# Optimization experiments

Measured on AMD Instinct MI355X. Metric: run time of the kernel, lower is better.

## Reference

```python
import jax, jax.numpy as jnp
import numpy as np

B, H, LB, PW, TC = 4096, 64, 32, 16, 1
WL = LB + PW  # window_length = look_back + prediction


def setup_inputs() -> dict:
    key = jax.random.key(0)
    ks = jax.random.split(key, 9)
    bnd = 1.0 / np.sqrt(H)  # torch Linear default init bound
    bnd_h = 1.0 / np.sqrt(H)
    return {
        "x": jax.random.normal(ks[0], (B, LB, TC), jnp.float32),
        "F_w": jax.random.uniform(ks[1], (WL, H, H), jnp.float32, -bnd, bnd),
        "F_b": jax.random.uniform(ks[2], (WL, H), jnp.float32, -bnd, bnd),
        "H_w": jax.random.uniform(ks[3], (WL, TC, H), jnp.float32, -bnd_h, bnd_h),
        "H_b": jax.random.uniform(ks[4], (WL, TC), jnp.float32, -bnd_h, bnd_h),
        "initial_state": jax.random.normal(ks[5], (H,), jnp.float32),
        "initial_covariance": 0.1 * jax.random.normal(ks[6], (H, H), jnp.float32),
        "Q": 0.1 * jax.random.normal(ks[7], (H, H), jnp.float32),
        "R": jnp.eye(TC, dtype=jnp.float32) + 0.1 * jax.random.normal(ks[8], (TC, TC), jnp.float32),
    }


def _kalman_forward(x, F_w, F_b, H_w, H_b, s0, P0, Q, R):
    nb = x.shape[0]
    hs = jnp.broadcast_to(s0, (nb, H))          # (B,H)
    P = jnp.broadcast_to(P0, (nb, H, H))        # (B,H,H)
    ys = jnp.moveaxis(x[:, :LB, :TC], 0, 1)     # (LB,B,TC) per-step observations

    @jax.checkpoint
    def kf_step(carry, inp):
        hs, P = carry
        Fw, Fb, Hw, Hb, y = inp
        hs_pred = hs @ Fw.T + Fb                                        # (B,H)
        P_pred = jnp.einsum('ij,bjk,lk->bil', Fw, P, Fw) + Q            # F P F^T + Q
        resid = y - (hs_pred @ Hw.T + Hb)                               # (B,TC)
        S = jnp.einsum('ij,bjk,lk->bil', Hw, P_pred, Hw) + R            # (B,TC,TC)
        K = jnp.einsum('bij,kj->bik', P_pred, Hw) @ jnp.linalg.inv(S)   # (B,H,TC)
        hs_new = hs_pred + jnp.einsum('bij,bj->bi', K, resid)
        P_new = P_pred - jnp.einsum('bit,tj,bjk->bik', K, Hw, P_pred)   # (I-KH)P_pred
        return (hs_new, P_new), None

    (hs, _), _ = jax.lax.scan(
        kf_step, (hs, P), (F_w[:LB], F_b[:LB], H_w[:LB], H_b[:LB], ys))

    def pred_step(hs, inp):
        Fw, Fb, Hw, Hb = inp
        hs = hs @ Fw.T + Fb
        return hs, hs @ Hw.T + Hb

    _, ems = jax.lax.scan(
        pred_step, hs, (F_w[LB:], F_b[LB:], H_w[LB:], H_b[LB:]))  # (PW,B,TC)
    # torch.cat(preds, dim=1).unsqueeze(-1) -> (B, PW*TC, 1)
    return jnp.moveaxis(ems, 0, 1).reshape(nb, PW * TC)[..., None]


def reference(x, F_w, F_b, H_w, H_b, initial_state, initial_covariance, Q, R):
    return _kalman_forward(x, F_w, F_b, H_w, H_b, initial_state, initial_covariance, Q, R)
```

## Files before the change

kernel.cpp:

```cpp
#include <hip/hip_runtime.h>


constexpr int KP_OFF = 0;
constexpr int WP_OFF = 2048;
constexpr int UP_OFF = 4160;
constexpr int EP_OFF = 5184;
constexpr int WS_U64 = 5200;

typedef float    f32x4 __attribute__((ext_vector_type(4)));
typedef _Float16 f16x4 __attribute__((ext_vector_type(4)));
typedef _Float16 f16x8 __attribute__((ext_vector_type(8)));

#define MFMA16(a, b, c) __builtin_amdgcn_mfma_f32_16x16x16f16((a), (b), (c), 0, 0, 0)

template <int CTRL>
__device__ __forceinline__ float dpp_add(float x) {
  int v = __builtin_amdgcn_update_dpp(0, __builtin_bit_cast(int, x), CTRL, 0xf, 0xf, true);
  return x + __builtin_bit_cast(float, v);
}
__device__ __forceinline__ float sum16(float x) {
  x = dpp_add<0xB1>(x);
  x = dpp_add<0x4E>(x);
  x = dpp_add<0x141>(x);
  x = dpp_add<0x140>(x);
  return x;
}
__device__ __forceinline__ float sum64(float x) {
  x = sum16(x);
  x += __shfl_xor(x, 16, 64);
  x += __shfl_xor(x, 32, 64);
  return x;
}

__device__ __forceinline__ float spin_read(const unsigned long long* p, unsigned tag) {
  unsigned long long v = 0;
  for (int it = 0; it < (1 << 22); ++it) {
    v = __hip_atomic_load(p, __ATOMIC_RELAXED, __HIP_MEMORY_SCOPE_AGENT);
    if ((unsigned)(v >> 32) == tag) break;
  }
  union { unsigned u; float f; } cv; cv.u = (unsigned)v;
  return cv.f;
}
__device__ __forceinline__ void pub_write(unsigned long long* p, unsigned tag, float x) {
  union { float f; unsigned u; } cv; cv.f = x;
  __hip_atomic_store(p, ((unsigned long long)tag << 32) | cv.u,
                     __ATOMIC_RELAXED, __HIP_MEMORY_SCOPE_AGENT);
}

__global__ __launch_bounds__(512) void kalman_fused(
    const float* __restrict__ Fw, const float* __restrict__ Fb,
    const float* __restrict__ Hw, const float* __restrict__ Hb,
    const float* __restrict__ s0, const float* __restrict__ P0,
    const float* __restrict__ Qg, const float* __restrict__ Rg,
    const float* __restrict__ x, float* __restrict__ out,
    unsigned long long* __restrict__ ws) {
  __shared__ __align__(16) char smem[55040];
  const int tid  = threadIdx.x;
  const int lane = tid & 63;
  const int w    = tid >> 6;
  const int blk  = blockIdx.x;
  unsigned long long* kp = ws + KP_OFF;
  unsigned long long* wp = ws + WP_OFF;
  unsigned long long* up = ws + UP_OFF;
  unsigned long long* ep = ws + EP_OFF;

  if (blk == 0) {
    _Float16* FF  = (_Float16*)smem;
    _Float16* TF  = (_Float16*)(smem + 16640);
    float*    PF  = (float*)(smem + 33024);
    float*    nred = (float*)(smem + 53504);
    float*    mred = (float*)(smem + 54016);

    const int l15 = lane & 15, g = lane >> 4;
    const int ti = w >> 1, half = w & 1;
    const int lp0 = 16 * (l15 >> 2) + 4 * g;
    const int rg  = l15 & 3;
    const int sr = tid >> 3, sc0 = (tid & 7) * 8;
    const int fi = (sr >> 4) * 4 + (sc0 >> 4);
    const int L0 = (sr & 15) + 16 * ((sc0 >> 2) & 3);
    const float R0 = Rg[0];

    auto FFp = [&](int f, int l) { return FF + (f * 65 + l) * 8; };
    auto TFp = [&](int f, int l) { return TF + (f * 64 + l) * 8; };
    auto PFi = [&](int f, int l, int r) { return (f * 64 + l) * 5 + r; };

    auto stageF = [&](f32x4 a, f32x4 b) {
      f16x8 pa, pb;
      #pragma unroll
      for (int u = 0; u < 4; ++u) {
        const _Float16 ha = (_Float16)a[u];
        pa[u] = ha; pa[4 + u] = (_Float16)((a[u] - (float)ha) * 2048.0f);
        const _Float16 hb = (_Float16)b[u];
        pb[u] = hb; pb[4 + u] = (_Float16)((b[u] - (float)hb) * 2048.0f);
      }
      *(f16x8*)FFp(fi, L0)      = pa;
      *(f16x8*)FFp(fi, L0 + 16) = pb;
    };

    float qf0[4], qf1[4];
    #pragma unroll
    for (int reg = 0; reg < 4; ++reg) {
      qf0[reg] = Qg[(16 * ti + 4 * g + reg) * 64 + 16 * (2 * half) + l15];
      qf1[reg] = Qg[(16 * ti + 4 * g + reg) * 64 + 16 * (2 * half + 1) + l15];
    }
    #pragma unroll
    for (int u = 0; u < 8; ++u) {
      const int cc = sc0 + u;
      PF[PFi((sr >> 4) * 4 + (cc >> 4), 16 * ((sr & 15) >> 2) + (cc & 15), sr & 3)] =
          P0[sr * 64 + cc];
    }
    f32x4 fpa = *(const f32x4*)(Fw + sr * 64 + sc0);
    f32x4 fpb = *(const f32x4*)(Fw + sr * 64 + sc0 + 4);
    stageF(fpa, fpb);
    float hcur = Hw[lane], hprev = 0.f, hnext = 0.f;
    __syncthreads();

    for (int t = 0; t < 32; ++t) {
      float kv = 0.f, mr = 0.f;
      if (t > 0) {
        const float n = nred[lane] + nred[64 + lane];
        mr = mred[lane] + mred[64 + lane] + mred[128 + lane] + mred[192 + lane];
        const float s = sum64(hprev * n);
        kv = n / (s + R0);
        if (w == 0) pub_write(&kp[(t - 1) * 64 + lane], (unsigned)t, kv);
      }
      if (t + 1 < 32) {
        fpa = *(const f32x4*)(Fw + (size_t)(t + 1) * 4096 + sr * 64 + sc0);
        fpb = *(const f32x4*)(Fw + (size_t)(t + 1) * 4096 + sr * 64 + sc0 + 4);
        hnext = Hw[(t + 1) * 64 + lane];
      }
      const float kr = __shfl(kv, l15 + 16 * ti, 64);
      f16x4 Ah[4], Al[4];
      #pragma unroll
      for (int kc = 0; kc < 4; ++kc) {
        #pragma unroll
        for (int j = 0; j < 4; ++j) {
          const float mcol = __shfl(mr, 16 * kc + 4 * g + j, 64);
          const float pv = PF[PFi(ti * 4 + kc, lp0 + j, rg)] - kr * mcol;
          const _Float16 hi_ = (_Float16)pv;
          Ah[kc][j] = hi_;
          Al[kc][j] = (_Float16)((pv - (float)hi_) * 2048.0f);
        }
      }
      f16x4 FAh[4], FAl[4];
      #pragma unroll
      for (int kc = 0; kc < 4; ++kc) {
        const f16x8 av = *(const f16x8*)FFp(ti * 4 + kc, lane);
        FAh[kc] = __builtin_shufflevector(av, av, 0, 1, 2, 3);
        FAl[kc] = __builtin_shufflevector(av, av, 4, 5, 6, 7);
      }
      #pragma unroll
      for (int s2 = 0; s2 < 2; ++s2) {
        const int tj = 2 * half + s2;
        f32x4 am = {0.f, 0.f, 0.f, 0.f}, a1 = {0.f, 0.f, 0.f, 0.f}, a2 = {0.f, 0.f, 0.f, 0.f};
        #pragma unroll
        for (int kc = 0; kc < 4; ++kc) {
          const f16x8 bv = *(const f16x8*)FFp(tj * 4 + kc, lane);
          const f16x4 bh = __builtin_shufflevector(bv, bv, 0, 1, 2, 3);
          const f16x4 bl = __builtin_shufflevector(bv, bv, 4, 5, 6, 7);
          am = MFMA16(Ah[kc], bh, am);
          a1 = MFMA16(Ah[kc], bl, a1);
          a2 = MFMA16(Al[kc], bh, a2);
        }
        const f32x4 outv = am + (a1 + a2) * (1.0f / 2048.0f);
        f16x8 tv;
        #pragma unroll
        for (int j = 0; j < 4; ++j) {
          const _Float16 hi_ = (_Float16)outv[j];
          tv[j] = hi_;
          tv[4 + j] = (_Float16)((outv[j] - (float)hi_) * 2048.0f);
        }
        *(f16x8*)TFp(ti * 4 + tj, lane) = tv;
      }
      __syncthreads();

      if (t + 1 < 32) stageF(fpa, fpb);
      f32x4 pout[2];
      #pragma unroll
      for (int s2 = 0; s2 < 2; ++s2) {
        const int tj = 2 * half + s2;
        f32x4 am = {0.f, 0.f, 0.f, 0.f}, a1 = {0.f, 0.f, 0.f, 0.f}, a2 = {0.f, 0.f, 0.f, 0.f};
        #pragma unroll
        for (int kc = 0; kc < 4; ++kc) {
          const f16x8 bv = *(const f16x8*)TFp(kc * 4 + tj, lane);
          const f16x4 bh = __builtin_shufflevector(bv, bv, 0, 1, 2, 3);
          const f16x4 bl = __builtin_shufflevector(bv, bv, 4, 5, 6, 7);
          am = MFMA16(FAh[kc], bh, am);
          a1 = MFMA16(FAh[kc], bl, a1);
          a2 = MFMA16(FAl[kc], bh, a2);
        }
        pout[s2] = am + (a1 + a2) * (1.0f / 2048.0f);
        #pragma unroll
        for (int reg = 0; reg < 4; ++reg) {
          pout[s2][reg] += (s2 ? qf1[reg] : qf0[reg]);
          PF[PFi(ti * 4 + tj, lane, reg)] = pout[s2][reg];
        }
      }
      const float hcA = __shfl(hcur, 16 * (2 * half) + l15, 64);
      const float hcB = __shfl(hcur, 16 * (2 * half + 1) + l15, 64);
      float hr[4];
      #pragma unroll
      for (int reg = 0; reg < 4; ++reg) hr[reg] = __shfl(hcur, 16 * ti + 4 * g + reg, 64);
      #pragma unroll
      for (int reg = 0; reg < 4; ++reg) {
        float np = pout[0][reg] * hcA + pout[1][reg] * hcB;
        np = sum16(np);
        if (l15 == 0) nred[half * 64 + 16 * ti + 4 * g + reg] = np;
      }
      float mp0 = 0.f, mp1 = 0.f;
      #pragma unroll
      for (int reg = 0; reg < 4; ++reg) {
        mp0 += pout[0][reg] * hr[reg];
        mp1 += pout[1][reg] * hr[reg];
      }
      mp0 += __shfl_xor(mp0, 16, 64); mp0 += __shfl_xor(mp0, 32, 64);
      mp1 += __shfl_xor(mp1, 16, 64); mp1 += __shfl_xor(mp1, 32, 64);
      if (g == 0) {
        mred[ti * 64 + 16 * (2 * half) + l15]     = mp0;
        mred[ti * 64 + 16 * (2 * half + 1) + l15] = mp1;
      }
      __syncthreads();
      hprev = hcur; hcur = hnext;
    }
    {
      const float n = nred[lane] + nred[64 + lane];
      const float s = sum64(hprev * n);
      if (w == 0) pub_write(&kp[31 * 64 + lane], 32u, n / (s + R0));
    }
    return;
  }

  if (blk == 1) {
    for (int pi = 0; pi < 2; ++pi) {
      const int p = pi ? (15 - w) : w;
      const int q = 32 + p;
      float r = Hw[q * 64 + lane];
      float eacc = 0.f;
      for (int s = 0; s <= p; ++s) {
        const int m = q - s;
        eacc += r * Fb[m * 64 + lane];
        const float* Fm = Fw + (size_t)m * 4096;
        float r0 = 0.f, r1 = 0.f, r2 = 0.f, r3 = 0.f;
        for (int j = 0; j < 64; j += 4) {
          r0 += __shfl(r, j,     64) * Fm[j * 64 + lane];
          r1 += __shfl(r, j + 1, 64) * Fm[(j + 1) * 64 + lane];
          r2 += __shfl(r, j + 2, 64) * Fm[(j + 2) * 64 + lane];
          r3 += __shfl(r, j + 3, 64) * Fm[(j + 3) * 64 + lane];
        }
        r = (r0 + r1) + (r2 + r3);
      }
      eacc = sum64(eacc);
      pub_write(&up[p * 64 + lane], 1u, r);
      if (lane == 0) pub_write(&ep[p], 1u, eacc + Hb[q]);
    }
    return;
  }

  if (blk < 7) {
    float* vb = (float*)smem + w * 64;
    const int c = (blk - 2) * 8 + w;
    if (c > 32) return;
    if (c == 32) {
      pub_write(&wp[32 * 64 + lane], 1u, spin_read(&kp[31 * 64 + lane], 32u));
      return;
    }
    const int t0 = (c == 0) ? 0 : c;
    float v = (c == 0) ? s0[lane] : spin_read(&kp[(c - 1) * 64 + lane], (unsigned)c);
    f32x4 fn[16];
    {
      const float* Fr = Fw + (size_t)t0 * 4096 + lane * 64;
      #pragma unroll
      for (int jc = 0; jc < 16; ++jc) fn[jc] = *(const f32x4*)(Fr + jc * 4);
    }
    float hn  = Hw[t0 * 64 + lane];
    float fbn = (c == 0) ? Fb[t0 * 64 + lane] : 0.f;
    for (int t = t0; t < 32; ++t) {
      vb[lane] = v;
      f32x4 fc[16];
      #pragma unroll
      for (int jc = 0; jc < 16; ++jc) fc[jc] = fn[jc];
      const float ht = hn, fbt = fbn;
      if (t + 1 < 32) {
        const float* Fr = Fw + (size_t)(t + 1) * 4096 + lane * 64;
        #pragma unroll
        for (int jc = 0; jc < 16; ++jc) fn[jc] = *(const f32x4*)(Fr + jc * 4);
        hn = Hw[(t + 1) * 64 + lane];
        if (c == 0) fbn = Fb[(t + 1) * 64 + lane];
      }
      float a0 = fbt, a1 = 0.f, a2 = 0.f, a3 = 0.f;
      #pragma unroll
      for (int jc = 0; jc < 16; ++jc) {
        const f32x4 vv = *(const f32x4*)(vb + jc * 4);
        a0 += fc[jc].x * vv.x; a1 += fc[jc].y * vv.y;
        a2 += fc[jc].z * vv.z; a3 += fc[jc].w * vv.w;
      }
      const float vp = (a0 + a1) + (a2 + a3);
      float hv = sum64(ht * vp);
      if (c == 0) hv += Hb[t];
      const float kt = spin_read(&kp[t * 64 + lane], (unsigned)(t + 1));
      v = vp - kt * hv;
    }
    pub_write(&wp[c * 64 + lane], 1u, v);
    return;
  }

  {
    float* Ul = (float*)smem;
    float* Wl = (float*)(smem + 4352);
    float* Zl = (float*)(smem + 13328);
    float* El = (float*)(smem + 15504);
    for (int idx = tid; idx < 1024; idx += 512)
      Ul[(idx >> 6) * 68 + (idx & 63)] = spin_read(&up[idx], 1u);
    for (int idx = tid; idx < 2112; idx += 512)
      Wl[(idx >> 6) * 68 + (idx & 63)] = spin_read(&wp[idx], 1u);
    if (tid < 16) El[tid] = spin_read(&ep[tid], 1u);
    __syncthreads();
    for (int idx = tid; idx < 528; idx += 512) {
      const int p = idx / 33, cc = idx - p * 33;
      const float* Up = Ul + p * 68;
      const float* Wc = Wl + cc * 68;
      float a0 = 0.f, a1 = 0.f, a2 = 0.f, a3 = 0.f;
      #pragma unroll 4
      for (int i = 0; i < 64; i += 4) {
        a0 += Up[i] * Wc[i];     a1 += Up[i + 1] * Wc[i + 1];
        a2 += Up[i + 2] * Wc[i + 2]; a3 += Up[i + 3] * Wc[i + 3];
      }
      float z = (a0 + a1) + (a2 + a3);
      if (cc == 0) z += El[p];
      Zl[p * 34 + cc] = z;
    }
    const int b = (blk - 7) * 512 + tid;
    f32x4 xr[8];
    const f32x4* xp = (const f32x4*)(x + (size_t)b * 32);
    #pragma unroll
    for (int u = 0; u < 8; ++u) xr[u] = xp[u];
    __syncthreads();
    float acc[16];
    #pragma unroll
    for (int p = 0; p < 16; ++p) acc[p] = Zl[p * 34];
    #pragma unroll
    for (int u = 0; u < 8; ++u) {
      #pragma unroll
      for (int e = 0; e < 4; ++e) {
        const float xval = xr[u][e];
        const int t = u * 4 + e;
        #pragma unroll
        for (int p = 0; p < 16; ++p) acc[p] += Zl[p * 34 + 1 + t] * xval;
      }
    }
    float4* op = (float4*)(out + (size_t)b * 16);
    op[0] = make_float4(acc[0], acc[1], acc[2], acc[3]);
    op[1] = make_float4(acc[4], acc[5], acc[6], acc[7]);
    op[2] = make_float4(acc[8], acc[9], acc[10], acc[11]);
    op[3] = make_float4(acc[12], acc[13], acc[14], acc[15]);
  }
}

extern "C" void kernel_launch(void* const* d_in, const int* in_sizes, int n_in,
                              void* d_out, int out_size, void* d_ws, size_t ws_size,
                              hipStream_t stream) {
  (void)in_sizes; (void)n_in; (void)out_size; (void)ws_size;
  const float* x  = (const float*)d_in[0];
  const float* Fw = (const float*)d_in[1];
  const float* Fb = (const float*)d_in[2];
  const float* Hw = (const float*)d_in[3];
  const float* Hb = (const float*)d_in[4];
  const float* s0 = (const float*)d_in[5];
  const float* P0 = (const float*)d_in[6];
  const float* Q  = (const float*)d_in[7];
  const float* R  = (const float*)d_in[8];
  float* out = (float*)d_out;
  unsigned long long* ws = (unsigned long long*)d_ws;

  hipMemsetAsync(d_ws, 0, WS_U64 * sizeof(unsigned long long), stream);
  kalman_fused<<<15, 512, 0, stream>>>(Fw, Fb, Hw, Hb, s0, P0, Q, R, x, out, ws);
}
```

Measured before the change: 127.7 us.

## Fold per-column state recurrence into covariance block via MFMA, drop cross-block spin

Moves the 33 column-vector propagation chains out of five separate blocks, which spun on per-step Kalman gains, and into block 0. Two of its waves compute them together with split-fp16 MFMA against the staged F. This removes the per-timestep cross-block atomic handshakes and cuts the grid from 15 to 10 blocks. It also replaces __syncthreads with a lightweight LDS barrier and adds sleep-based completion flags, so consumer blocks prefetch x before waiting. The cost is extra MFMA and shuffle work on block 0's critical path, plus fp16 hi/lo precision in the vector path.

```diff
diff --git a/kernel.cpp b/kernel.cpp
--- a/kernel.cpp
+++ b/kernel.cpp
@@ -1,11 +1,11 @@
 #include <hip/hip_runtime.h>
 
 
-constexpr int KP_OFF = 0;
-constexpr int WP_OFF = 2048;
-constexpr int UP_OFF = 4160;
-constexpr int EP_OFF = 5184;
-constexpr int WS_U64 = 5200;
+constexpr int WP_OFF = 0;
+constexpr int UP_OFF = 2112;
+constexpr int EP_OFF = 3136;
+constexpr int FL_OFF = 3152;
+constexpr int WS_U64 = 3154;
 
 typedef float    f32x4 __attribute__((ext_vector_type(4)));
 typedef _Float16 f16x4 __attribute__((ext_vector_type(4)));
@@ -45,6 +45,19 @@
   union { float f; unsigned u; } cv; cv.f = x;
   __hip_atomic_store(p, ((unsigned long long)tag << 32) | cv.u,
                      __ATOMIC_RELAXED, __HIP_MEMORY_SCOPE_AGENT);
+}
+__device__ __forceinline__ void wait_flag(const unsigned long long* p, unsigned tag) {
+  for (int it = 0; it < (1 << 20); ++it) {
+    if ((unsigned)(__hip_atomic_load(p, __ATOMIC_RELAXED, __HIP_MEMORY_SCOPE_AGENT) >> 32) == tag)
+      return;
+    __builtin_amdgcn_s_sleep(16);
+  }
+}
+__device__ __forceinline__ void lds_barrier() {
+  asm volatile("s_waitcnt lgkmcnt(0)" ::: "memory");
+  __builtin_amdgcn_sched_barrier(0);
+  __builtin_amdgcn_s_barrier();
+  __builtin_amdgcn_sched_barrier(0);
 }
 
 __global__ __launch_bounds__(512) void kalman_fused(
@@ -59,7 +72,6 @@
   const int lane = tid & 63;
   const int w    = tid >> 6;
   const int blk  = blockIdx.x;
-  unsigned long long* kp = ws + KP_OFF;
   unsigned long long* wp = ws + WP_OFF;
   unsigned long long* up = ws + UP_OFF;
   unsigned long long* ep = ws + EP_OFF;
@@ -79,6 +91,8 @@
     const int fi = (sr >> 4) * 4 + (sc0 >> 4);
     const int L0 = (sr & 15) + 16 * ((sc0 >> 2) & 3);
     const float R0 = Rg[0];
+    const bool isV = (w < 2);
+    const int ct = w;
 
     auto FFp = [&](int f, int l) { return FF + (f * 65 + l) * 8; };
     auto TFp = [&](int f, int l) { return TF + (f * 64 + l) * 8; };
@@ -113,21 +127,74 @@
     f32x4 fpb = *(const f32x4*)(Fw + sr * 64 + sc0 + 4);
     stageF(fpa, fpb);
     float hcur = Hw[lane], hprev = 0.f, hnext = 0.f;
+    float fbcur = Fb[lane], fbnext = 0.f;
+    float hbcur = Hb[0], hbnext = 0.f;
+
+    const float s0v = s0[lane];
+    f16x4 VbH[4], VbL[4];
+    #pragma unroll
+    for (int kc = 0; kc < 4; ++kc)
+      #pragma unroll
+      for (int j = 0; j < 4; ++j) {
+        const float sv = __shfl(s0v, 16 * kc + 4 * g + j, 64);
+        const float v = (ct == 0 && l15 == 0) ? sv : 0.f;
+        const _Float16 h_ = (_Float16)v;
+        VbH[kc][j] = h_;
+        VbL[kc][j] = (_Float16)((v - (float)h_) * 2048.0f);
+      }
+    f32x4 vpv[4];
+    float qreg = 0.f;
     __syncthreads();
 
     for (int t = 0; t < 32; ++t) {
+      if (t + 1 < 32) {
+        fpa = *(const f32x4*)(Fw + (size_t)(t + 1) * 4096 + sr * 64 + sc0);
+        fpb = *(const f32x4*)(Fw + (size_t)(t + 1) * 4096 + sr * 64 + sc0 + 4);
+        hnext  = Hw[(t + 1) * 64 + lane];
+        fbnext = Fb[(t + 1) * 64 + lane];
+        hbnext = Hb[t + 1];
+      }
       float kv = 0.f, mr = 0.f;
       if (t > 0) {
         const float n = nred[lane] + nred[64 + lane];
         mr = mred[lane] + mred[64 + lane] + mred[128 + lane] + mred[192 + lane];
         const float s = sum64(hprev * n);
         kv = n / (s + R0);
-        if (w == 0) pub_write(&kp[(t - 1) * 64 + lane], (unsigned)t, kv);
-      }
-      if (t + 1 < 32) {
-        fpa = *(const f32x4*)(Fw + (size_t)(t + 1) * 4096 + sr * 64 + sc0);
-        fpb = *(const f32x4*)(Fw + (size_t)(t + 1) * 4096 + sr * 64 + sc0 + 4);
-        hnext = Hw[(t + 1) * 64 + lane];
+      }
+      if (isV) {
+        if (t > 0) {
+          #pragma unroll
+          for (int rt = 0; rt < 4; ++rt)
+            #pragma unroll
+            for (int j = 0; j < 4; ++j) {
+              const float kr2 = __shfl(kv, 16 * rt + 4 * g + j, 64);
+              float val = vpv[rt][j] - kr2 * qreg;
+              if (l15 == t - 16 * ct) val = kr2;
+              const _Float16 h_ = (_Float16)val;
+              VbH[rt][j] = h_;
+              VbL[rt][j] = (_Float16)((val - (float)h_) * 2048.0f);
+            }
+        }
+        #pragma unroll
+        for (int rt = 0; rt < 4; ++rt) {
+          f32x4 am, a1;
+          #pragma unroll
+          for (int r = 0; r < 4; ++r) {
+            const float bsh = __shfl(fbcur, 16 * rt + 4 * g + r, 64);
+            am[r] = (ct == 0 && l15 == 0) ? bsh : 0.f;
+            a1[r] = 0.f;
+          }
+          #pragma unroll
+          for (int kc = 0; kc < 4; ++kc) {
+            const f16x8 av = *(const f16x8*)FFp(rt * 4 + kc, lane);
+            const f16x4 ah = __builtin_shufflevector(av, av, 0, 1, 2, 3);
+            const f16x4 al = __builtin_shufflevector(av, av, 4, 5, 6, 7);
+            am = MFMA16(ah, VbH[kc], am);
+            a1 = MFMA16(ah, VbL[kc], a1);
+            a1 = MFMA16(al, VbH[kc], a1);
+          }
+          vpv[rt] = am + a1 * (1.0f / 2048.0f);
+        }
       }
       const float kr = __shfl(kv, l15 + 16 * ti, 64);
       f16x4 Ah[4], Al[4];
@@ -137,9 +204,9 @@
         for (int j = 0; j < 4; ++j) {
           const float mcol = __shfl(mr, 16 * kc + 4 * g + j, 64);
           const float pv = PF[PFi(ti * 4 + kc, lp0 + j, rg)] - kr * mcol;
-          const _Float16 hi_ = (_Float16)pv;
-          Ah[kc][j] = hi_;
-          Al[kc][j] = (_Float16)((pv - (float)hi_) * 2048.0f);
+          const _Float16 h_ = (_Float16)pv;
+          Ah[kc][j] = h_;
+          Al[kc][j] = (_Float16)((pv - (float)h_) * 2048.0f);
         }
       }
       f16x4 FAh[4], FAl[4];
@@ -166,13 +233,13 @@
         f16x8 tv;
         #pragma unroll
         for (int j = 0; j < 4; ++j) {
-          const _Float16 hi_ = (_Float16)outv[j];
-          tv[j] = hi_;
-          tv[4 + j] = (_Float16)((outv[j] - (float)hi_) * 2048.0f);
+          const _Float16 h_ = (_Float16)outv[j];
+          tv[j] = h_;
+          tv[4 + j] = (_Float16)((outv[j] - (float)h_) * 2048.0f);
         }
         *(f16x8*)TFp(ti * 4 + tj, lane) = tv;
       }
-      __syncthreads();
+      lds_barrier();
 
       if (t + 1 < 32) stageF(fpa, fpb);
       f32x4 pout[2];
@@ -219,14 +286,40 @@
         mred[ti * 64 + 16 * (2 * half) + l15]     = mp0;
         mred[ti * 64 + 16 * (2 * half + 1) + l15] = mp1;
       }
-      __syncthreads();
-      hprev = hcur; hcur = hnext;
-    }
+      if (isV) {
+        float qp = 0.f;
+        #pragma unroll
+        for (int rt = 0; rt < 4; ++rt)
+          #pragma unroll
+          for (int r = 0; r < 4; ++r)
+            qp += __shfl(hcur, 16 * rt + 4 * g + r, 64) * vpv[rt][r];
+        qp += __shfl_xor(qp, 16, 64);
+        qp += __shfl_xor(qp, 32, 64);
+        if (ct == 0 && l15 == 0) qp += hbcur;
+        qreg = qp;
+      }
+      lds_barrier();
+      hprev = hcur; hcur = hnext; fbcur = fbnext; hbcur = hbnext;
+    }
+
     {
       const float n = nred[lane] + nred[64 + lane];
       const float s = sum64(hprev * n);
-      if (w == 0) pub_write(&kp[31 * 64 + lane], 32u, n / (s + R0));
-    }
+      const float k31 = n / (s + R0);
+      if (isV) {
+        #pragma unroll
+        for (int rt = 0; rt < 4; ++rt)
+          #pragma unroll
+          for (int j = 0; j < 4; ++j) {
+            const float kr2 = __shfl(k31, 16 * rt + 4 * g + j, 64);
+            const float val = vpv[rt][j] - kr2 * qreg;
+            pub_write(&wp[(16 * ct + l15) * 64 + 16 * rt + 4 * g + j], 1u, val);
+          }
+      }
+      if (w == 2) pub_write(&wp[32 * 64 + lane], 1u, k31);
+    }
+    __syncthreads();
+    if (tid == 0) pub_write(&ws[FL_OFF], 1u, 0.f);
     return;
   }
 
@@ -253,54 +346,8 @@
       pub_write(&up[p * 64 + lane], 1u, r);
       if (lane == 0) pub_write(&ep[p], 1u, eacc + Hb[q]);
     }
-    return;
-  }
-
-  if (blk < 7) {
-    float* vb = (float*)smem + w * 64;
-    const int c = (blk - 2) * 8 + w;
-    if (c > 32) return;
-    if (c == 32) {
-      pub_write(&wp[32 * 64 + lane], 1u, spin_read(&kp[31 * 64 + lane], 32u));
-      return;
-    }
-    const int t0 = (c == 0) ? 0 : c;
-    float v = (c == 0) ? s0[lane] : spin_read(&kp[(c - 1) * 64 + lane], (unsigned)c);
-    f32x4 fn[16];
-    {
-      const float* Fr = Fw + (size_t)t0 * 4096 + lane * 64;
-      #pragma unroll
-      for (int jc = 0; jc < 16; ++jc) fn[jc] = *(const f32x4*)(Fr + jc * 4);
-    }
-    float hn  = Hw[t0 * 64 + lane];
-    float fbn = (c == 0) ? Fb[t0 * 64 + lane] : 0.f;
-    for (int t = t0; t < 32; ++t) {
-      vb[lane] = v;
-      f32x4 fc[16];
-      #pragma unroll
-      for (int jc = 0; jc < 16; ++jc) fc[jc] = fn[jc];
-      const float ht = hn, fbt = fbn;
-      if (t + 1 < 32) {
-        const float* Fr = Fw + (size_t)(t + 1) * 4096 + lane * 64;
-        #pragma unroll
-        for (int jc = 0; jc < 16; ++jc) fn[jc] = *(const f32x4*)(Fr + jc * 4);
-        hn = Hw[(t + 1) * 64 + lane];
-        if (c == 0) fbn = Fb[(t + 1) * 64 + lane];
-      }
-      float a0 = fbt, a1 = 0.f, a2 = 0.f, a3 = 0.f;
-      #pragma unroll
-      for (int jc = 0; jc < 16; ++jc) {
-        const f32x4 vv = *(const f32x4*)(vb + jc * 4);
-        a0 += fc[jc].x * vv.x; a1 += fc[jc].y * vv.y;
-        a2 += fc[jc].z * vv.z; a3 += fc[jc].w * vv.w;
-      }
-      const float vp = (a0 + a1) + (a2 + a3);
-      float hv = sum64(ht * vp);
-      if (c == 0) hv += Hb[t];
-      const float kt = spin_read(&kp[t * 64 + lane], (unsigned)(t + 1));
-      v = vp - kt * hv;
-    }
-    pub_write(&wp[c * 64 + lane], 1u, v);
+    __syncthreads();
+    if (tid == 0) pub_write(&ws[FL_OFF + 1], 1u, 0.f);
     return;
   }
 
@@ -309,6 +356,17 @@
     float* Wl = (float*)(smem + 4352);
     float* Zl = (float*)(smem + 13328);
     float* El = (float*)(smem + 15504);
+    const int b = (blk - 2) * 512 + tid;
+    f32x4 xr[8];
+    const f32x4* xp = (const f32x4*)(x + (size_t)b * 32);
+    #pragma unroll
+    for (int u = 0; u < 8; ++u) xr[u] = xp[u];
+
+    if (tid == 0) {
+      wait_flag(&ws[FL_OFF], 1u);
+      wait_flag(&ws[FL_OFF + 1], 1u);
+    }
+    __syncthreads();
     for (int idx = tid; idx < 1024; idx += 512)
       Ul[(idx >> 6) * 68 + (idx & 63)] = spin_read(&up[idx], 1u);
     for (int idx = tid; idx < 2112; idx += 512)
@@ -322,18 +380,13 @@
       float a0 = 0.f, a1 = 0.f, a2 = 0.f, a3 = 0.f;
       #pragma unroll 4
       for (int i = 0; i < 64; i += 4) {
-        a0 += Up[i] * Wc[i];     a1 += Up[i + 1] * Wc[i + 1];
+        a0 += Up[i] * Wc[i];         a1 += Up[i + 1] * Wc[i + 1];
         a2 += Up[i + 2] * Wc[i + 2]; a3 += Up[i + 3] * Wc[i + 3];
       }
       float z = (a0 + a1) + (a2 + a3);
       if (cc == 0) z += El[p];
       Zl[p * 34 + cc] = z;
     }
-    const int b = (blk - 7) * 512 + tid;
-    f32x4 xr[8];
-    const f32x4* xp = (const f32x4*)(x + (size_t)b * 32);
-    #pragma unroll
-    for (int u = 0; u < 8; ++u) xr[u] = xp[u];
     __syncthreads();
     float acc[16];
     #pragma unroll
@@ -373,5 +426,5 @@
   unsigned long long* ws = (unsigned long long*)d_ws;
 
   hipMemsetAsync(d_ws, 0, WS_U64 * sizeof(unsigned long long), stream);
-  kalman_fused<<<15, 512, 0, stream>>>(Fw, Fb, Hw, Hb, s0, P0, Q, R, x, out, ws);
-}
+  kalman_fused<<<10, 512, 0, stream>>>(Fw, Fb, Hw, Hb, s0, P0, Q, R, x, out, ws);
+}
```

New measurement: 128.7 us. No clear change (+0.8%).

## Reduce covariance recursion precision, restructure Kalman gain reduction, add sleep-based completion counter

Applied to the files above, without the earlier changes.

The serial covariance block now stores F and the intermediate product in single fp16 instead of hi/lo split fp16, which cuts the MFMA count per step (2+1 instead of 3+3). The innovation scalar S is computed by a cross-wave reduction through LDS instead of a full-wave shuffle. P is stored in a vectorised layout, H rows are cached in LDS, and barriers are replaced by a lighter waitcnt plus s_barrier. Spinning consumers now sleep between polls, and the output blocks wait on a single completion counter with sleep before reading the published values, so fewer polling waves compete with the producers. The lower precision risks accuracy loss in P over the 32 steps.

```diff
diff --git a/kernel.cpp b/kernel.cpp
--- a/kernel.cpp
+++ b/kernel.cpp
@@ -5,11 +5,11 @@
 constexpr int WP_OFF = 2048;
 constexpr int UP_OFF = 4160;
 constexpr int EP_OFF = 5184;
-constexpr int WS_U64 = 5200;
+constexpr int CNT_OFF = 5200;
+constexpr int WS_U64 = 5201;
 
 typedef float    f32x4 __attribute__((ext_vector_type(4)));
 typedef _Float16 f16x4 __attribute__((ext_vector_type(4)));
-typedef _Float16 f16x8 __attribute__((ext_vector_type(8)));
 
 #define MFMA16(a, b, c) __builtin_amdgcn_mfma_f32_16x16x16f16((a), (b), (c), 0, 0, 0)
 
@@ -25,12 +25,6 @@
   x = dpp_add<0x140>(x);
   return x;
 }
-__device__ __forceinline__ float sum64(float x) {
-  x = sum16(x);
-  x += __shfl_xor(x, 16, 64);
-  x += __shfl_xor(x, 32, 64);
-  return x;
-}
 
 __device__ __forceinline__ float spin_read(const unsigned long long* p, unsigned tag) {
   unsigned long long v = 0;
@@ -41,10 +35,26 @@
   union { unsigned u; float f; } cv; cv.u = (unsigned)v;
   return cv.f;
 }
+__device__ __forceinline__ float spin_read_sleep(const unsigned long long* p, unsigned tag) {
+  unsigned long long v = 0;
+  for (int it = 0; it < (1 << 20); ++it) {
+    v = __hip_atomic_load(p, __ATOMIC_RELAXED, __HIP_MEMORY_SCOPE_AGENT);
+    if ((unsigned)(v >> 32) == tag) break;
+    __builtin_amdgcn_s_sleep(2);
+  }
+  union { unsigned u; float f; } cv; cv.u = (unsigned)v;
+  return cv.f;
+}
 __device__ __forceinline__ void pub_write(unsigned long long* p, unsigned tag, float x) {
   union { float f; unsigned u; } cv; cv.f = x;
   __hip_atomic_store(p, ((unsigned long long)tag << 32) | cv.u,
                      __ATOMIC_RELAXED, __HIP_MEMORY_SCOPE_AGENT);
+}
+__device__ __forceinline__ void lds_barrier() {
+  asm volatile("s_waitcnt lgkmcnt(0)" ::: "memory");
+  __builtin_amdgcn_sched_barrier(0);
+  __builtin_amdgcn_s_barrier();
+  __builtin_amdgcn_sched_barrier(0);
 }
 
 __global__ __launch_bounds__(512) void kalman_fused(
@@ -54,7 +64,7 @@
     const float* __restrict__ Qg, const float* __restrict__ Rg,
     const float* __restrict__ x, float* __restrict__ out,
     unsigned long long* __restrict__ ws) {
-  __shared__ __align__(16) char smem[55040];
+  __shared__ __align__(16) char smem[43008];
   const int tid  = threadIdx.x;
   const int lane = tid & 63;
   const int w    = tid >> 6;
@@ -65,167 +75,164 @@
   unsigned long long* ep = ws + EP_OFF;
 
   if (blk == 0) {
-    _Float16* FF  = (_Float16*)smem;
-    _Float16* TF  = (_Float16*)(smem + 16640);
-    float*    PF  = (float*)(smem + 33024);
-    float*    nred = (float*)(smem + 53504);
-    float*    mred = (float*)(smem + 54016);
+    _Float16* FFh = (_Float16*)smem;
+    _Float16* TF  = (_Float16*)(smem + 8192);
+    float*    PF  = (float*)(smem + 16384);
+    float*    Hws = (float*)(smem + 32768);
+    float*    nred = (float*)(smem + 40960);
+    float*    mred = (float*)(smem + 41472);
+    float*    Sred = (float*)(smem + 42496);
 
     const int l15 = lane & 15, g = lane >> 4;
     const int ti = w >> 1, half = w & 1;
-    const int lp0 = 16 * (l15 >> 2) + 4 * g;
-    const int rg  = l15 & 3;
+    const int tj0 = 2 * half, tj1 = 2 * half + 1;
     const int sr = tid >> 3, sc0 = (tid & 7) * 8;
-    const int fi = (sr >> 4) * 4 + (sc0 >> 4);
-    const int L0 = (sr & 15) + 16 * ((sc0 >> 2) & 3);
+    const int fi0 = (sr >> 4) * 4 + (sc0 >> 4);
+    const int L0  = (sr & 15) + 16 * ((sc0 & 15) >> 2);
     const float R0 = Rg[0];
 
-    auto FFp = [&](int f, int l) { return FF + (f * 65 + l) * 8; };
-    auto TFp = [&](int f, int l) { return TF + (f * 64 + l) * 8; };
-    auto PFi = [&](int f, int l, int r) { return (f * 64 + l) * 5 + r; };
-
-    auto stageF = [&](f32x4 a, f32x4 b) {
-      f16x8 pa, pb;
-      #pragma unroll
-      for (int u = 0; u < 4; ++u) {
-        const _Float16 ha = (_Float16)a[u];
-        pa[u] = ha; pa[4 + u] = (_Float16)((a[u] - (float)ha) * 2048.0f);
-        const _Float16 hb = (_Float16)b[u];
-        pb[u] = hb; pb[4 + u] = (_Float16)((b[u] - (float)hb) * 2048.0f);
-      }
-      *(f16x8*)FFp(fi, L0)      = pa;
-      *(f16x8*)FFp(fi, L0 + 16) = pb;
+    auto stageFh = [&](f32x4 a, f32x4 b) {
+      f16x4 pa, pb;
+      #pragma unroll
+      for (int u = 0; u < 4; ++u) { pa[u] = (_Float16)a[u]; pb[u] = (_Float16)b[u]; }
+      *(f16x4*)&FFh[(fi0 * 64 + L0) * 4]      = pa;
+      *(f16x4*)&FFh[(fi0 * 64 + L0 + 16) * 4] = pb;
     };
 
-    float qf0[4], qf1[4];
+    f32x4 qf0, qf1;
     #pragma unroll
     for (int reg = 0; reg < 4; ++reg) {
-      qf0[reg] = Qg[(16 * ti + 4 * g + reg) * 64 + 16 * (2 * half) + l15];
-      qf1[reg] = Qg[(16 * ti + 4 * g + reg) * 64 + 16 * (2 * half + 1) + l15];
-    }
+      qf0[reg] = Qg[(16 * ti + 4 * g + reg) * 64 + 16 * tj0 + l15];
+      qf1[reg] = Qg[(16 * ti + 4 * g + reg) * 64 + 16 * tj1 + l15];
+    }
+    for (int idx = tid; idx < 2048; idx += 512) Hws[idx] = Hw[idx];
     #pragma unroll
-    for (int u = 0; u < 8; ++u) {
-      const int cc = sc0 + u;
-      PF[PFi((sr >> 4) * 4 + (cc >> 4), 16 * ((sr & 15) >> 2) + (cc & 15), sr & 3)] =
-          P0[sr * 64 + cc];
-    }
-    f32x4 fpa = *(const f32x4*)(Fw + sr * 64 + sc0);
-    f32x4 fpb = *(const f32x4*)(Fw + sr * 64 + sc0 + 4);
-    stageF(fpa, fpb);
-    float hcur = Hw[lane], hprev = 0.f, hnext = 0.f;
+    for (int s = 0; s < 2; ++s) {
+      const int slot = tid + s * 512;
+      const int f = slot >> 6, ln = slot & 63;
+      const int a = f >> 2, b = f & 3, g2 = ln >> 4, l2 = ln & 15;
+      f32x4 v;
+      #pragma unroll
+      for (int r = 0; r < 4; ++r)
+        v[r] = P0[(16 * a + 4 * g2 + r) * 64 + 16 * b + l2];
+      *(f32x4*)&PF[(f * 64 + ln) * 4] = v;
+    }
+    {
+      f32x4 a = *(const f32x4*)(Fw + sr * 64 + sc0);
+      f32x4 b = *(const f32x4*)(Fw + sr * 64 + sc0 + 4);
+      stageFh(a, b);
+    }
+    for (int idx = tid; idx < 2 * 64; idx += 512) nred[idx] = 0.f;
+    for (int idx = tid; idx < 4 * 64; idx += 512) mred[idx] = 0.f;
+    if (tid < 8) Sred[tid] = 0.f;
     __syncthreads();
 
+    f32x4 fna, fnb;
     for (int t = 0; t < 32; ++t) {
-      float kv = 0.f, mr = 0.f;
-      if (t > 0) {
-        const float n = nred[lane] + nred[64 + lane];
-        mr = mred[lane] + mred[64 + lane] + mred[128 + lane] + mred[192 + lane];
-        const float s = sum64(hprev * n);
-        kv = n / (s + R0);
-        if (w == 0) pub_write(&kp[(t - 1) * 64 + lane], (unsigned)t, kv);
-      }
       if (t + 1 < 32) {
-        fpa = *(const f32x4*)(Fw + (size_t)(t + 1) * 4096 + sr * 64 + sc0);
-        fpb = *(const f32x4*)(Fw + (size_t)(t + 1) * 4096 + sr * 64 + sc0 + 4);
-        hnext = Hw[(t + 1) * 64 + lane];
-      }
-      const float kr = __shfl(kv, l15 + 16 * ti, 64);
+        fna = *(const f32x4*)(Fw + (size_t)(t + 1) * 4096 + sr * 64 + sc0);
+        fnb = *(const f32x4*)(Fw + (size_t)(t + 1) * 4096 + sr * 64 + sc0 + 4);
+      }
+      float S;
+      {
+        const f32x4 sa = *(const f32x4*)&Sred[0];
+        const f32x4 sb = *(const f32x4*)&Sred[4];
+        S = ((sa.x + sa.y) + (sa.z + sa.w)) + ((sb.x + sb.y) + (sb.z + sb.w));
+      }
+      const float rcpS = 1.0f / (S + R0);
+      const int ia = 16 * ti + l15;
+      const float hPl = mred[ia] + mred[64 + ia] + mred[128 + ia] + mred[192 + ia];
+
       f16x4 Ah[4], Al[4];
       #pragma unroll
       for (int kc = 0; kc < 4; ++kc) {
+        const int na = 16 * kc + 4 * g;
+        const f32x4 n4 = *(const f32x4*)&nred[na] + *(const f32x4*)&nred[64 + na];
+        const f32x4 k4 = n4 * rcpS;
+        const f32x4 p4 = *(const f32x4*)&PF[((kc * 4 + ti) * 64 + lane) * 4] - k4 * hPl;
         #pragma unroll
         for (int j = 0; j < 4; ++j) {
-          const float mcol = __shfl(mr, 16 * kc + 4 * g + j, 64);
-          const float pv = PF[PFi(ti * 4 + kc, lp0 + j, rg)] - kr * mcol;
-          const _Float16 hi_ = (_Float16)pv;
-          Ah[kc][j] = hi_;
-          Al[kc][j] = (_Float16)((pv - (float)hi_) * 2048.0f);
+          const _Float16 h_ = (_Float16)p4[j];
+          Ah[kc][j] = h_;
+          Al[kc][j] = (_Float16)((p4[j] - (float)h_) * 2048.0f);
         }
       }
-      f16x4 FAh[4], FAl[4];
-      #pragma unroll
-      for (int kc = 0; kc < 4; ++kc) {
-        const f16x8 av = *(const f16x8*)FFp(ti * 4 + kc, lane);
-        FAh[kc] = __builtin_shufflevector(av, av, 0, 1, 2, 3);
-        FAl[kc] = __builtin_shufflevector(av, av, 4, 5, 6, 7);
-      }
+      f16x4 Bf[2][4];
       #pragma unroll
       for (int s2 = 0; s2 < 2; ++s2) {
-        const int tj = 2 * half + s2;
-        f32x4 am = {0.f, 0.f, 0.f, 0.f}, a1 = {0.f, 0.f, 0.f, 0.f}, a2 = {0.f, 0.f, 0.f, 0.f};
+        const int tj = tj0 + s2;
+        #pragma unroll
+        for (int kc = 0; kc < 4; ++kc)
+          Bf[s2][kc] = *(const f16x4*)&FFh[((tj * 4 + kc) * 64 + lane) * 4];
+      }
+      if (w == 0 && t > 0) {
+        const float kl = (nred[lane] + nred[64 + lane]) * rcpS;
+        pub_write(&kp[(t - 1) * 64 + lane], (unsigned)t, kl);
+      }
+      #pragma unroll
+      for (int s2 = 0; s2 < 2; ++s2) {
+        const int tj = tj0 + s2;
+        f32x4 am = {0.f, 0.f, 0.f, 0.f}, a2 = {0.f, 0.f, 0.f, 0.f};
         #pragma unroll
         for (int kc = 0; kc < 4; ++kc) {
-          const f16x8 bv = *(const f16x8*)FFp(tj * 4 + kc, lane);
-          const f16x4 bh = __builtin_shufflevector(bv, bv, 0, 1, 2, 3);
-          const f16x4 bl = __builtin_shufflevector(bv, bv, 4, 5, 6, 7);
-          am = MFMA16(Ah[kc], bh, am);
-          a1 = MFMA16(Ah[kc], bl, a1);
-          a2 = MFMA16(Al[kc], bh, a2);
+          am = MFMA16(Ah[kc], Bf[s2][kc], am);
+          a2 = MFMA16(Al[kc], Bf[s2][kc], a2);
         }
-        const f32x4 outv = am + (a1 + a2) * (1.0f / 2048.0f);
-        f16x8 tv;
-        #pragma unroll
-        for (int j = 0; j < 4; ++j) {
-          const _Float16 hi_ = (_Float16)outv[j];
-          tv[j] = hi_;
-          tv[4 + j] = (_Float16)((outv[j] - (float)hi_) * 2048.0f);
-        }
-        *(f16x8*)TFp(ti * 4 + tj, lane) = tv;
-      }
-      __syncthreads();
-
-      if (t + 1 < 32) stageF(fpa, fpb);
+        const f32x4 uv = am + a2 * (1.0f / 2048.0f);
+        f16x4 uh;
+        #pragma unroll
+        for (int j = 0; j < 4; ++j) uh[j] = (_Float16)uv[j];
+        *(f16x4*)&TF[((ti * 4 + tj) * 64 + lane) * 4] = uh;
+      }
+      lds_barrier();
+
+      if (t + 1 < 32) stageFh(fna, fnb);
+      f16x4 Ua[4];
+      #pragma unroll
+      for (int kc = 0; kc < 4; ++kc)
+        Ua[kc] = *(const f16x4*)&TF[((kc * 4 + ti) * 64 + lane) * 4];
       f32x4 pout[2];
       #pragma unroll
       for (int s2 = 0; s2 < 2; ++s2) {
-        const int tj = 2 * half + s2;
-        f32x4 am = {0.f, 0.f, 0.f, 0.f}, a1 = {0.f, 0.f, 0.f, 0.f}, a2 = {0.f, 0.f, 0.f, 0.f};
-        #pragma unroll
-        for (int kc = 0; kc < 4; ++kc) {
-          const f16x8 bv = *(const f16x8*)TFp(kc * 4 + tj, lane);
-          const f16x4 bh = __builtin_shufflevector(bv, bv, 0, 1, 2, 3);
-          const f16x4 bl = __builtin_shufflevector(bv, bv, 4, 5, 6, 7);
-          am = MFMA16(FAh[kc], bh, am);
-          a1 = MFMA16(FAh[kc], bl, a1);
-          a2 = MFMA16(FAl[kc], bh, a2);
-        }
-        pout[s2] = am + (a1 + a2) * (1.0f / 2048.0f);
-        #pragma unroll
-        for (int reg = 0; reg < 4; ++reg) {
-          pout[s2][reg] += (s2 ? qf1[reg] : qf0[reg]);
-          PF[PFi(ti * 4 + tj, lane, reg)] = pout[s2][reg];
-        }
-      }
-      const float hcA = __shfl(hcur, 16 * (2 * half) + l15, 64);
-      const float hcB = __shfl(hcur, 16 * (2 * half + 1) + l15, 64);
-      float hr[4];
-      #pragma unroll
-      for (int reg = 0; reg < 4; ++reg) hr[reg] = __shfl(hcur, 16 * ti + 4 * g + reg, 64);
-      #pragma unroll
-      for (int reg = 0; reg < 4; ++reg) {
-        float np = pout[0][reg] * hcA + pout[1][reg] * hcB;
-        np = sum16(np);
-        if (l15 == 0) nred[half * 64 + 16 * ti + 4 * g + reg] = np;
-      }
-      float mp0 = 0.f, mp1 = 0.f;
-      #pragma unroll
-      for (int reg = 0; reg < 4; ++reg) {
-        mp0 += pout[0][reg] * hr[reg];
-        mp1 += pout[1][reg] * hr[reg];
-      }
+        const int tj = tj0 + s2;
+        f32x4 acc = {0.f, 0.f, 0.f, 0.f};
+        #pragma unroll
+        for (int kc = 0; kc < 4; ++kc) acc = MFMA16(Ua[kc], Bf[s2][kc], acc);
+        acc += (s2 ? qf1 : qf0);
+        pout[s2] = acc;
+        *(f32x4*)&PF[((ti * 4 + tj) * 64 + lane) * 4] = acc;
+      }
+      const float hcA = Hws[t * 64 + 16 * tj0 + l15];
+      const float hcB = Hws[t * 64 + 16 * tj1 + l15];
+      const f32x4 h4 = *(const f32x4*)&Hws[t * 64 + 16 * ti + 4 * g];
+      const f32x4 npv = pout[0] * hcA + pout[1] * hcB;
+      const float np0 = sum16(npv.x), np1 = sum16(npv.y);
+      const float np2 = sum16(npv.z), np3 = sum16(npv.w);
+      float sel = np0;
+      sel = (l15 == 1) ? np1 : sel;
+      sel = (l15 == 2) ? np2 : sel;
+      sel = (l15 == 3) ? np3 : sel;
+      if (l15 < 4) nred[half * 64 + 16 * ti + 4 * g + l15] = sel;
+      float mp0 = pout[0].x * h4.x + pout[0].y * h4.y + pout[0].z * h4.z + pout[0].w * h4.w;
+      float mp1 = pout[1].x * h4.x + pout[1].y * h4.y + pout[1].z * h4.z + pout[1].w * h4.w;
       mp0 += __shfl_xor(mp0, 16, 64); mp0 += __shfl_xor(mp0, 32, 64);
       mp1 += __shfl_xor(mp1, 16, 64); mp1 += __shfl_xor(mp1, 32, 64);
       if (g == 0) {
-        mred[ti * 64 + 16 * (2 * half) + l15]     = mp0;
-        mred[ti * 64 + 16 * (2 * half + 1) + l15] = mp1;
-      }
-      __syncthreads();
-      hprev = hcur; hcur = hnext;
-    }
-    {
-      const float n = nred[lane] + nred[64 + lane];
-      const float s = sum64(hprev * n);
-      if (w == 0) pub_write(&kp[31 * 64 + lane], 32u, n / (s + R0));
+        mred[ti * 64 + 16 * tj0 + l15] = mp0;
+        mred[ti * 64 + 16 * tj1 + l15] = mp1;
+      }
+      float sp = npv.x * h4.x + npv.y * h4.y + npv.z * h4.z + npv.w * h4.w;
+      sp = sum16(sp);
+      sp += __shfl_xor(sp, 16, 64); sp += __shfl_xor(sp, 32, 64);
+      if (lane == 0) Sred[w] = sp;
+      lds_barrier();
+    }
+    if (w == 0) {
+      const f32x4 sa = *(const f32x4*)&Sred[0];
+      const f32x4 sb = *(const f32x4*)&Sred[4];
+      const float S = ((sa.x + sa.y) + (sa.z + sa.w)) + ((sb.x + sb.y) + (sb.z + sb.w));
+      const float kl = (nred[lane] + nred[64 + lane]) / (S + R0);
+      pub_write(&kp[31 * 64 + lane], 32u, kl);
     }
     return;
   }
@@ -249,10 +256,14 @@
         }
         r = (r0 + r1) + (r2 + r3);
       }
-      eacc = sum64(eacc);
+      eacc = sum16(eacc);
+      eacc += __shfl_xor(eacc, 16, 64); eacc += __shfl_xor(eacc, 32, 64);
       pub_write(&up[p * 64 + lane], 1u, r);
       if (lane == 0) pub_write(&ep[p], 1u, eacc + Hb[q]);
     }
+    __syncthreads();
+    if (tid == 0)
+      __hip_atomic_fetch_add(&ws[CNT_OFF], 1ull, __ATOMIC_RELAXED, __HIP_MEMORY_SCOPE_AGENT);
     return;
   }
 
@@ -261,11 +272,13 @@
     const int c = (blk - 2) * 8 + w;
     if (c > 32) return;
     if (c == 32) {
-      pub_write(&wp[32 * 64 + lane], 1u, spin_read(&kp[31 * 64 + lane], 32u));
+      pub_write(&wp[32 * 64 + lane], 1u, spin_read_sleep(&kp[31 * 64 + lane], 32u));
+      if (lane == 0)
+        __hip_atomic_fetch_add(&ws[CNT_OFF], 1ull, __ATOMIC_RELAXED, __HIP_MEMORY_SCOPE_AGENT);
       return;
     }
     const int t0 = (c == 0) ? 0 : c;
-    float v = (c == 0) ? s0[lane] : spin_read(&kp[(c - 1) * 64 + lane], (unsigned)c);
+    float v = (c == 0) ? s0[lane] : spin_read_sleep(&kp[(c - 1) * 64 + lane], (unsigned)c);
     f32x4 fn[16];
     {
       const float* Fr = Fw + (size_t)t0 * 4096 + lane * 64;
@@ -295,12 +308,16 @@
         a2 += fc[jc].z * vv.z; a3 += fc[jc].w * vv.w;
       }
       const float vp = (a0 + a1) + (a2 + a3);
-      float hv = sum64(ht * vp);
+      float hv = ht * vp;
+      hv = sum16(hv);
+      hv += __shfl_xor(hv, 16, 64); hv += __shfl_xor(hv, 32, 64);
       if (c == 0) hv += Hb[t];
-      const float kt = spin_read(&kp[t * 64 + lane], (unsigned)(t + 1));
+      const float kt = spin_read_sleep(&kp[t * 64 + lane], (unsigned)(t + 1));
       v = vp - kt * hv;
     }
     pub_write(&wp[c * 64 + lane], 1u, v);
+    if (lane == 0)
+      __hip_atomic_fetch_add(&ws[CNT_OFF], 1ull, __ATOMIC_RELAXED, __HIP_MEMORY_SCOPE_AGENT);
     return;
   }
 
@@ -309,6 +326,20 @@
     float* Wl = (float*)(smem + 4352);
     float* Zl = (float*)(smem + 13328);
     float* El = (float*)(smem + 15504);
+    const int b = (blk - 7) * 512 + tid;
+    f32x4 xr[8];
+    const f32x4* xp = (const f32x4*)(x + (size_t)b * 32);
+    #pragma unroll
+    for (int u = 0; u < 8; ++u) xr[u] = xp[u];
+
+    if (tid == 0) {
+      for (int it = 0; it < (1 << 20); ++it) {
+        if (__hip_atomic_load(&ws[CNT_OFF], __ATOMIC_RELAXED, __HIP_MEMORY_SCOPE_AGENT) >= 34ull)
+          break;
+        __builtin_amdgcn_s_sleep(8);
+      }
+    }
+    __syncthreads();
     for (int idx = tid; idx < 1024; idx += 512)
       Ul[(idx >> 6) * 68 + (idx & 63)] = spin_read(&up[idx], 1u);
     for (int idx = tid; idx < 2112; idx += 512)
@@ -322,18 +353,13 @@
       float a0 = 0.f, a1 = 0.f, a2 = 0.f, a3 = 0.f;
       #pragma unroll 4
       for (int i = 0; i < 64; i += 4) {
-        a0 += Up[i] * Wc[i];     a1 += Up[i + 1] * Wc[i + 1];
+        a0 += Up[i] * Wc[i];         a1 += Up[i + 1] * Wc[i + 1];
         a2 += Up[i + 2] * Wc[i + 2]; a3 += Up[i + 3] * Wc[i + 3];
       }
       float z = (a0 + a1) + (a2 + a3);
       if (cc == 0) z += El[p];
       Zl[p * 34 + cc] = z;
     }
-    const int b = (blk - 7) * 512 + tid;
-    f32x4 xr[8];
-    const f32x4* xp = (const f32x4*)(x + (size_t)b * 32);
-    #pragma unroll
-    for (int u = 0; u < 8; ++u) xr[u] = xp[u];
     __syncthreads();
     float acc[16];
     #pragma unroll
```

After: 128.9 us. No clear change (+0.9%).
